# Kernel optimization log

Measured on AMD Instinct MI355X. Metric: run time of the kernel, lower is better.

Reference implementation:

```python
import jax, jax.numpy as jnp
import numpy as np

B, S, D = 128, 256, 768          # batch, seq (pre-sentinel), encoder dim
ARC, TAG = 500, 100              # arc / tag representation dims
LAYERS, TOPK = 2, 8              # config['gnn_layers'], config['top_k']
SP = S + 1                       # seq_len after head sentinel


def setup_inputs() -> dict:
    key = jax.random.key(0)
    ks = jax.random.split(key, 32)
    sc = 0.02
    inp = {
        'inputs': jax.random.normal(ks[0], (B, S, D), jnp.float32),
        'tag_embeddings': jax.random.randint(ks[1], (B, S), 0, 50),
        'mask': jnp.ones((B, S), jnp.int32),
        'head_indices': jax.random.randint(ks[2], (B, S), 0, S),
        'head_tags': jax.random.randint(ks[3], (B, S), 0, 50),
        # parameters
        'head_sentinel': jax.random.normal(ks[4], (D,), jnp.float32),
        'W_ha': jax.random.normal(ks[5], (D, ARC)) * sc, 'b_ha': jnp.zeros((ARC,)),
        'W_da': jax.random.normal(ks[6], (D, ARC)) * sc, 'b_da': jnp.zeros((ARC,)),
        'W_ht': jax.random.normal(ks[7], (D, TAG)) * sc, 'b_ht': jnp.zeros((TAG,)),
        'W_dt': jax.random.normal(ks[8], (D, TAG)) * sc, 'b_dt': jnp.zeros((TAG,)),
        # bilinear attention: use_input_biases=True -> (ARC+1, ARC+1), plus scalar bias
        'bil_W': jax.random.normal(ks[9], (LAYERS + 1, ARC + 1, ARC + 1)) * sc,
        'bil_b': jnp.zeros((LAYERS + 1,)),
        # GCNConv params (PyG: x @ W, symmetric-normalized aggregate, + bias)
        'c1a_W': jax.random.normal(ks[10], (ARC, ARC)) * sc, 'c1a_b': jnp.zeros((ARC,)),
        'c2a_W': jax.random.normal(ks[11], (ARC, ARC)) * sc, 'c2a_b': jnp.zeros((ARC,)),
        'c1r_W': jax.random.normal(ks[12], (TAG, TAG)) * sc, 'c1r_b': jnp.zeros((TAG,)),
        'c2r_W': jax.random.normal(ks[13], (TAG, TAG)) * sc, 'c2r_b': jnp.zeros((TAG,)),
    }
    return inp


def bilinear_attn(m1, m2, W, b):
    # AllenNLP BilinearMatrixAttention with use_input_biases=True
    ones1 = jnp.ones(m1.shape[:-1] + (1,), m1.dtype)
    m1b = jnp.concatenate([m1, ones1], -1)
    m2b = jnp.concatenate([m2, ones1], -1)
    return jnp.einsum('bie,ef,bjf->bij', m1b, W, m2b) + b


def batch_top_k(probs, k):
    # probs: [B, SP, SP] row-softmaxed; edge j(head)->i(dep) for each row's top-k cols,
    # with global (batched) node indexing.
    vals, idx = jax.lax.top_k(probs, k)                      # [B, SP, k]
    offs = (jnp.arange(B) * SP)[:, None, None]
    src = (idx + offs).reshape(-1)
    dst = (jnp.broadcast_to(jnp.arange(SP)[None, :, None], idx.shape) + offs).reshape(-1)
    return src, dst, vals.reshape(-1)


def gcn_conv(x, src, dst, ew, W, b):
    # PyG GCNConv: x@W, add self-loops (weight 1), sym norm, scatter-add at dst, + bias
    N = x.shape[0]
    x = x @ W
    loop = jnp.arange(N)
    row = jnp.concatenate([src, loop])
    col = jnp.concatenate([dst, loop])
    w = jnp.concatenate([ew, jnp.ones((N,), x.dtype)])
    deg = jax.ops.segment_sum(w, col, num_segments=N)
    dinv = jnp.where(deg > 0, jax.lax.rsqrt(deg), 0.0)
    norm = dinv[row] * w * dinv[col]
    out = jax.ops.segment_sum(x[row] * norm[:, None], col, num_segments=N)
    return out + b


def reference(inputs, tag_embeddings, mask, head_indices, head_tags,
              head_sentinel, W_ha, b_ha, W_da, b_da, W_ht, b_ht, W_dt, b_dt,
              bil_W, bil_b, c1a_W, c1a_b, c2a_W, c2a_b, c1r_W, c1r_b, c2r_W, c2r_b):
    elu = jax.nn.elu
    x = jnp.concatenate([jnp.broadcast_to(head_sentinel, (B, 1, D)), inputs], axis=1)  # [B,SP,D]
    head_arc = elu(x @ W_ha + b_ha)
    dept_arc = elu(x @ W_da + b_da)
    head_tag = elu(x @ W_ht + b_ht)
    dep_tag = elu(x @ W_dt + b_dt)

    def two_conv(feat, W1, b1, W2, b2, src, dst, ew):
        h = gcn_conv(feat.reshape(B * SP, -1), src, dst, ew, W1, b1)
        h = gcn_conv(elu(h), src, dst, ew, W2, b2)
        return h.reshape(B, SP, -1)

    for k in range(LAYERS):
        arc_logits = bilinear_attn(head_arc, dept_arc, bil_W[k], bil_b[k])
        arc_probs = jax.nn.softmax(arc_logits, axis=-1)
        src, dst, ew = batch_top_k(arc_probs, TOPK)
        head_arc = two_conv(head_arc, c1a_W, c1a_b, c2a_W, c2a_b, src, dst, ew)
        dept_arc = two_conv(dept_arc, c1a_W, c1a_b, c2a_W, c2a_b, src, dst, ew)
        head_tag = two_conv(head_tag, c1r_W, c1r_b, c2r_W, c2r_b, src, dst, ew)
        dep_tag = two_conv(dep_tag, c1r_W, c1r_b, c2r_W, c2r_b, src, dst, ew)

    arc_logits = bilinear_attn(head_arc, dept_arc, bil_W[-1], bil_b[-1])
    return arc_logits, head_tag, dep_tag
```

## Files before the change

kernel.cpp:

```cpp
#include <hip/hip_runtime.h>
#include <hip/hip_bf16.h>
#include <math.h>
#include <cstddef>

namespace {

constexpr int kB   = 128;
constexpr int kS   = 256;
constexpr int kD   = 768;
constexpr int kSP  = 257;
constexpr int kN   = kB * kSP;
constexpr int kARC = 500;
constexpr int kTAG = 100;
constexpr int KA   = 512;
constexpr int KT   = 128;

typedef __attribute__((ext_vector_type(8))) short short8;
typedef __attribute__((ext_vector_type(4))) float floatx4;
typedef __attribute__((ext_vector_type(2))) float floatx2;
typedef __attribute__((ext_vector_type(4))) unsigned short ushort4v;
typedef __attribute__((ext_vector_type(2))) unsigned short ushort2v;
typedef __hip_bfloat16 bf;

__device__ __forceinline__ float bfval(bf h) { return __bfloat162float(h); }
__device__ __forceinline__ unsigned short bfbits(bf h) {
  unsigned short u; __builtin_memcpy(&u, &h, 2); return u;
}
__device__ __forceinline__ void splitf(float x, bf* h, bf* l) {
  bf hh = __float2bfloat16(x);
  *h = hh;
  *l = __float2bfloat16(x - __bfloat162float(hh));
}

__device__ __forceinline__ void gload16(const bf* g, bf* l) {
  __builtin_amdgcn_global_load_lds(
      (const __attribute__((address_space(1))) void*)g,
      (__attribute__((address_space(3))) void*)l, 16, 0, 0);
}

__global__ void detect_dtype_n(const unsigned* __restrict__ raw, int* __restrict__ flag,
                               int nwords) {
  int lane = threadIdx.x;
  int ok = 0, nz = 0;
  if (lane < nwords) {
    unsigned w = raw[lane];
    if (w != 0u) {
      nz = 1;
      int e = (w >> 7) & 0xFF;
      ok = (e >= 90 && e <= 140);
    }
  }
  unsigned long long ball_ok = __ballot(ok);
  unsigned long long ball_nz = __ballot(nz);
  if (lane == 0) {
    int cok = __popcll(ball_ok), cnz = __popcll(ball_nz);
    flag[0] = (cok * 4 >= cnz * 3) ? 1 : 0;
  }
}

__device__ __forceinline__ float rawload(const void* p, size_t i, int bfm) {
  return bfm ? __bfloat162float(((const bf*)p)[i]) : ((const float*)p)[i];
}

__global__ void conv_off(const void* __restrict__ src, float* __restrict__ dst,
                         int n, long off, const int* __restrict__ flag) {
  int i = blockIdx.x * 256 + threadIdx.x;
  if (i >= n) return;
  dst[i] = rawload(src, (size_t)off + i, *flag);
}

__global__ void wsplit_t(const void* __restrict__ src, const int* __restrict__ flag,
                         long srcOff, int ldsrc, int K, int N, int Kpad,
                         bf* __restrict__ Wh, bf* __restrict__ Wl) {
  long idx = (long)blockIdx.x * 256 + threadIdx.x;
  if (idx >= (long)N * Kpad) return;
  int n = (int)(idx / Kpad), k = (int)(idx % Kpad);
  float v = (k < K) ? rawload(src, (size_t)srcOff + (size_t)k * ldsrc + n, *flag) : 0.f;
  bf h, l;
  splitf(v, &h, &l);
  Wh[idx] = h; Wl[idx] = l;
}

__global__ void xsplit(const void* __restrict__ inp, const void* __restrict__ sent,
                       const int* __restrict__ fi, const int* __restrict__ fs,
                       bf* __restrict__ xh, bf* __restrict__ xl, int g0, int NG) {
  long idx = (long)blockIdx.x * 256 + threadIdx.x;
  long tot = (long)NG * (kD / 4);
  if (idx >= tot) return;
  int n = (int)(idx / (kD / 4));
  int k = (int)(idx % (kD / 4)) * 4;
  int b = n / kSP, r = n - b * kSP;
  const void* src;
  size_t base;
  int bfm;
  if (r == 0) { src = sent; base = (size_t)k; bfm = *fs; }
  else {
    src = inp;
    base = ((size_t)((g0 + b) * kS + (r - 1))) * kD + k;
    bfm = *fi;
  }
  float v[4];
  if (bfm) {
    ushort4v s = *(const ushort4v*)((const unsigned short*)src + base);
#pragma unroll
    for (int j = 0; j < 4; ++j) {
      bf h; unsigned short u = s[j];
      __builtin_memcpy(&h, &u, 2);
      v[j] = __bfloat162float(h);
    }
  } else {
    floatx4 f4 = *(const floatx4*)((const float*)src + base);
#pragma unroll
    for (int j = 0; j < 4; ++j) v[j] = f4[j];
  }
  ushort4v h4, l4;
#pragma unroll
  for (int j = 0; j < 4; ++j) {
    bf h, l;
    splitf(v[j], &h, &l);
    h4[j] = bfbits(h); l4[j] = bfbits(l);
  }
  size_t o = (size_t)n * kD + k;
  *(ushort4v*)((unsigned short*)xh + o) = h4;
  *(ushort4v*)((unsigned short*)xl + o) = l4;
}

constexpr int BM = 128, BN = 128, BK = 32;

template <int EPI, int OUTF32>
__global__ __launch_bounds__(256) void gemm_sp(
    const bf* __restrict__ Ah, const bf* __restrict__ Al, int lda,
    const bf* __restrict__ Bh, const bf* __restrict__ Bl, int ldb,
    bf* __restrict__ Ch, bf* __restrict__ Cl, float* __restrict__ Cf, int ldc,
    int M, int N, int K, const float* __restrict__ bias) {
  __shared__ bf sAh[BM][BK];
  __shared__ bf sAl[BM][BK];
  __shared__ bf sBh[BN][BK];
  __shared__ bf sBl[BN][BK];
  const int tid = threadIdx.x;
  const int lane = tid & 63, wave = tid >> 6;
  const int quad = lane >> 4, l15 = lane & 15;
  const int wm = (wave >> 1) * 64, wn = (wave & 1) * 64;
  const int m0 = blockIdx.x * BM, n0 = blockIdx.y * BN;
  const int lrow = lane >> 2, lkof = (lane & 3) * 8;

  const bf *pAh[2], *pAl[2], *pBh[2], *pBl[2];
#pragma unroll
  for (int jj = 0; jj < 2; ++jj) {
    int rb = wave * 32 + jj * 16;
    int gm = m0 + rb + lrow; if (gm > M - 1) gm = M - 1;
    int gn = n0 + rb + lrow; if (gn > N - 1) gn = N - 1;
    pAh[jj] = Ah + (size_t)gm * lda + lkof;
    pAl[jj] = Al + (size_t)gm * lda + lkof;
    pBh[jj] = Bh + (size_t)gn * ldb + lkof;
    pBl[jj] = Bl + (size_t)gn * ldb + lkof;
  }

  floatx4 acc[4][4] = {};
  for (int k0 = 0; k0 < K; k0 += BK) {
#pragma unroll
    for (int jj = 0; jj < 2; ++jj) {
      const int rb = wave * 32 + jj * 16;
      gload16(pAh[jj] + k0, &sAh[rb][0]);
      gload16(pAl[jj] + k0, &sAl[rb][0]);
      gload16(pBh[jj] + k0, &sBh[rb][0]);
      gload16(pBl[jj] + k0, &sBl[rb][0]);
    }
    __syncthreads();
    short8 a_h[4], a_l[4], b_h[4], b_l[4];
#pragma unroll
    for (int t = 0; t < 4; ++t) {
      a_h[t] = *(const short8*)&sAh[wm + t * 16 + l15][quad * 8];
      a_l[t] = *(const short8*)&sAl[wm + t * 16 + l15][quad * 8];
      b_h[t] = *(const short8*)&sBh[wn + t * 16 + l15][quad * 8];
      b_l[t] = *(const short8*)&sBl[wn + t * 16 + l15][quad * 8];
    }
#pragma unroll
    for (int mt = 0; mt < 4; ++mt)
#pragma unroll
      for (int nt = 0; nt < 4; ++nt) {
        acc[mt][nt] = __builtin_amdgcn_mfma_f32_16x16x32_bf16(a_h[mt], b_h[nt], acc[mt][nt], 0, 0, 0);
        acc[mt][nt] = __builtin_amdgcn_mfma_f32_16x16x32_bf16(a_h[mt], b_l[nt], acc[mt][nt], 0, 0, 0);
        acc[mt][nt] = __builtin_amdgcn_mfma_f32_16x16x32_bf16(a_l[mt], b_h[nt], acc[mt][nt], 0, 0, 0);
      }
    __syncthreads();
  }
#pragma unroll
  for (int mt = 0; mt < 4; ++mt)
#pragma unroll
    for (int reg = 0; reg < 4; ++reg) {
      int m = m0 + wm + mt * 16 + quad * 4 + reg;
      if (m >= M) continue;
#pragma unroll
      for (int nt = 0; nt < 4; ++nt) {
        int n = n0 + wn + nt * 16 + l15;
        if (OUTF32) {
          if (n < N) {
            float v = acc[mt][nt][reg];
            if (EPI >= 1) v += bias[n];
            if (EPI == 1) v = v > 0.f ? v : expm1f(v);
            Cf[(size_t)m * ldc + n] = v;
          }
        } else {
          size_t o = (size_t)m * ldc + n;
          if (n < N) {
            float v = acc[mt][nt][reg];
            if (EPI >= 1) v += bias[n];
            if (EPI == 1) v = v > 0.f ? v : expm1f(v);
            bf h, l;
            splitf(v, &h, &l);
            Ch[o] = h; Cl[o] = l;
          } else if (n < ldc) {
            Ch[o] = __float2bfloat16(0.f);
            Cl[o] = __float2bfloat16(0.f);
          }
        }
      }
    }
}

__global__ __launch_bounds__(256) void bilnt_sp(
    const bf* __restrict__ Th, const bf* __restrict__ Tl,
    const bf* __restrict__ Fh, const bf* __restrict__ Fl,
    float* __restrict__ out, const float* __restrict__ bilb, int bidx,
    int g0, int globOut) {
  __shared__ bf sAh[BM][BK];
  __shared__ bf sAl[BM][BK];
  __shared__ bf sBh[BN][BK];
  __shared__ bf sBl[BN][BK];
  const int z = blockIdx.z;
  const int tid = threadIdx.x;
  const int lane = tid & 63, wave = tid >> 6;
  const int quad = lane >> 4, l15 = lane & 15;
  const int wm = (wave >> 1) * 64, wn = (wave & 1) * 64;
  const int m0 = blockIdx.x * BM, n0 = blockIdx.y * BN;
  const int lrow = lane >> 2, lkof = (lane & 3) * 8;
  const bf* Ah = Th + (size_t)z * kSP * KA;
  const bf* Al = Tl + (size_t)z * kSP * KA;
  const bf* Bh = Fh + (size_t)z * kSP * KA;
  const bf* Bl = Fl + (size_t)z * kSP * KA;

  const bf *pAh[2], *pAl[2], *pBh[2], *pBl[2];
#pragma unroll
  for (int jj = 0; jj < 2; ++jj) {
    int rb = wave * 32 + jj * 16;
    int gm = m0 + rb + lrow; if (gm > kSP - 1) gm = kSP - 1;
    int gn = n0 + rb + lrow; if (gn > kSP - 1) gn = kSP - 1;
    pAh[jj] = Ah + (size_t)gm * KA + lkof;
    pAl[jj] = Al + (size_t)gm * KA + lkof;
    pBh[jj] = Bh + (size_t)gn * KA + lkof;
    pBl[jj] = Bl + (size_t)gn * KA + lkof;
  }

  floatx4 acc[4][4] = {};
  for (int k0 = 0; k0 < KA; k0 += BK) {
#pragma unroll
    for (int jj = 0; jj < 2; ++jj) {
      const int rb = wave * 32 + jj * 16;
      gload16(pAh[jj] + k0, &sAh[rb][0]);
      gload16(pAl[jj] + k0, &sAl[rb][0]);
      gload16(pBh[jj] + k0, &sBh[rb][0]);
      gload16(pBl[jj] + k0, &sBl[rb][0]);
    }
    __syncthreads();
    short8 a_h[4], a_l[4], b_h[4], b_l[4];
#pragma unroll
    for (int t = 0; t < 4; ++t) {
      a_h[t] = *(const short8*)&sAh[wm + t * 16 + l15][quad * 8];
      a_l[t] = *(const short8*)&sAl[wm + t * 16 + l15][quad * 8];
      b_h[t] = *(const short8*)&sBh[wn + t * 16 + l15][quad * 8];
      b_l[t] = *(const short8*)&sBl[wn + t * 16 + l15][quad * 8];
    }
#pragma unroll
    for (int mt = 0; mt < 4; ++mt)
#pragma unroll
      for (int nt = 0; nt < 4; ++nt) {
        acc[mt][nt] = __builtin_amdgcn_mfma_f32_16x16x32_bf16(a_h[mt], b_h[nt], acc[mt][nt], 0, 0, 0);
        acc[mt][nt] = __builtin_amdgcn_mfma_f32_16x16x32_bf16(a_h[mt], b_l[nt], acc[mt][nt], 0, 0, 0);
        acc[mt][nt] = __builtin_amdgcn_mfma_f32_16x16x32_bf16(a_l[mt], b_h[nt], acc[mt][nt], 0, 0, 0);
      }
    __syncthreads();
  }
  const float sb = bilb[bidx];
  const int bb = globOut ? (g0 + z) : z;
#pragma unroll
  for (int mt = 0; mt < 4; ++mt)
#pragma unroll
    for (int reg = 0; reg < 4; ++reg) {
      int i = m0 + wm + mt * 16 + quad * 4 + reg;
      if (i >= kSP) continue;
      float rowterm = bfval(Ah[(size_t)i * KA + 500]) + bfval(Al[(size_t)i * KA + 500]) + sb;
#pragma unroll
      for (int nt = 0; nt < 4; ++nt) {
        int j = n0 + wn + nt * 16 + l15;
        if (j >= kSP) continue;
        out[((size_t)bb * kSP + i) * kSP + j] = acc[mt][nt][reg] + rowterm;
      }
    }
}

__global__ void softmax_topk(const float* __restrict__ logits,
                             int* __restrict__ idx8,
                             float* __restrict__ val8,
                             float* __restrict__ dinv) {
  const int row = blockIdx.x;
  const int lane = threadIdx.x;
  const int rowbase = row - (row % kSP);
  const float* L = logits + (size_t)row * kSP;
  float v[5];
  int c[5];
#pragma unroll
  for (int q = 0; q < 5; ++q) {
    int j = lane + q * 64;
    c[q] = j;
    v[q] = (j < kSP) ? L[j] : -INFINITY;
  }
  float m = v[0];
#pragma unroll
  for (int q = 1; q < 5; ++q) m = fmaxf(m, v[q]);
  for (int off = 32; off > 0; off >>= 1) m = fmaxf(m, __shfl_xor(m, off));
  float s = 0.f;
#pragma unroll
  for (int q = 0; q < 5; ++q) s += expf(v[q] - m);
  for (int off = 32; off > 0; off >>= 1) s += __shfl_xor(s, off);
  const float invs = 1.f / s;
  float degsum = 0.f;
  for (int t = 0; t < 8; ++t) {
    float bvv = -INFINITY;
    int bii = kSP;
#pragma unroll
    for (int q = 0; q < 5; ++q)
      if (v[q] > bvv) { bvv = v[q]; bii = c[q]; }
    for (int off = 32; off > 0; off >>= 1) {
      float ov = __shfl_xor(bvv, off);
      int oi = __shfl_xor(bii, off);
      if (ov > bvv || (ov == bvv && oi < bii)) { bvv = ov; bii = oi; }
    }
    float p = expf(bvv - m) * invs;
    degsum += p;
    if (lane == 0) { idx8[row * 8 + t] = rowbase + bii; val8[row * 8 + t] = p; }
#pragma unroll
    for (int q = 0; q < 5; ++q)
      if (c[q] == bii) v[q] = -INFINITY;
  }
  if (lane == 0) dinv[row] = 1.f / sqrtf(1.f + degsum);
}

template <int ELU, int OUTF32>
__global__ void gcn_agg(const float* __restrict__ Y, int ldy, int F,
                        const int* __restrict__ idx8, const float* __restrict__ val8,
                        const float* __restrict__ dinv, const float* __restrict__ bias,
                        bf* __restrict__ Zh, bf* __restrict__ Zl,
                        float* __restrict__ Zf, int ldzf) {
  const int n = blockIdx.x;
  __shared__ float w[9];
  __shared__ int srcs[8];
  const int t = threadIdx.x;
  if (t < 8) {
    int s = idx8[n * 8 + t];
    srcs[t] = s;
    w[t] = dinv[n] * val8[n * 8 + t] * dinv[s];
  } else if (t == 8) {
    float di = dinv[n];
    w[8] = di * di;
  }
  __syncthreads();
  const int lim = OUTF32 ? F : ldy;
  for (int f = t * 2; f < lim; f += (int)blockDim.x * 2) {
    size_t on = (size_t)n * ldy + f;
    if (!OUTF32 && f >= F) {
      ushort2v zz = {0, 0};
      *(ushort2v*)((unsigned short*)Zh + on) = zz;
      *(ushort2v*)((unsigned short*)Zl + on) = zz;
      continue;
    }
    floatx2 y0 = *(const floatx2*)(Y + on);
    float a0 = w[8] * y0[0], a1 = w[8] * y0[1];
#pragma unroll
    for (int e = 0; e < 8; ++e) {
      floatx2 ys = *(const floatx2*)(Y + (size_t)srcs[e] * ldy + f);
      a0 += w[e] * ys[0];
      a1 += w[e] * ys[1];
    }
    a0 += bias[f];
    a1 += bias[f + 1];
    if (ELU) {
      a0 = a0 > 0.f ? a0 : expm1f(a0);
      a1 = a1 > 0.f ? a1 : expm1f(a1);
    }
    if (OUTF32) {
      floatx2 o = {a0, a1};
      *(floatx2*)(Zf + (size_t)n * ldzf + f) = o;
    } else {
      bf h0, l0, h1, l1;
      splitf(a0, &h0, &l0);
      splitf(a1, &h1, &l1);
      ushort2v hv = {bfbits(h0), bfbits(h1)};
      ushort2v lv = {bfbits(l0), bfbits(l1)};
      *(ushort2v*)((unsigned short*)Zh + on) = hv;
      *(ushort2v*)((unsigned short*)Zl + on) = lv;
    }
  }
}

}

extern "C" void kernel_launch(void* const* d_in, const int* in_sizes, int n_in,
                              void* d_out, int out_size, void* d_ws, size_t ws_size,
                              hipStream_t stream) {
  (void)out_size;

  const int roleSize[20] = {kB * kS * kD, kD,
                            kD * kARC, kARC, kD * kARC, kARC,
                            kD * kTAG, kTAG, kD * kTAG, kTAG,
                            3 * 501 * 501, 3,
                            kARC * kARC, kARC, kARC * kARC, kARC,
                            kTAG * kTAG, kTAG, kTAG * kTAG, kTAG};
  const int roleOcc[20]  = {0, 0, 0, 0, 1, 1, 0, 0, 1, 1, 0, 0,
                            0, 2, 1, 3, 0, 2, 1, 3};
  int roleIdx[20] = {0, 5, 6, 7, 8, 9, 10, 11, 12, 13, 14, 15,
                     16, 17, 18, 19, 20, 21, 22, 23};
  for (int r = 0; r < 20; ++r) {
    int occ = 0, found = -1;
    for (int i = 0; i < n_in; ++i) {
      if (in_sizes[i] == roleSize[r]) {
        if (occ == roleOcc[r]) { found = i; break; }
        ++occ;
      }
    }
    if (found >= 0) roleIdx[r] = found;
    else if (roleIdx[r] >= n_in) roleIdx[r] = 0;
  }
  const void* src_of[20];
  for (int r = 0; r < 20; ++r) src_of[r] = d_in[roleIdx[r]];

  auto need_bytes = [](int GB) -> size_t {
    size_t NG = (size_t)GB * kSP, s = 0;
    auto al = [&](size_t b) { s += (b + 255) & ~(size_t)255; };
    al(256);
    for (int i = 0; i < 4; ++i) al((size_t)kARC * kD * 2);
    for (int i = 0; i < 4; ++i) al((size_t)kTAG * kD * 2);
    al(kARC * 4); al(kARC * 4); al(kTAG * 4); al(kTAG * 4);
    for (int i = 0; i < 6; ++i) al((size_t)501 * KA * 2);
    al(3 * 501 * 4); al(256);
    for (int i = 0; i < 4; ++i) al((size_t)kARC * KA * 2);
    for (int i = 0; i < 4; ++i) al((size_t)kTAG * KT * 2);
    al(kARC * 4); al(kARC * 4); al(kTAG * 4); al(kTAG * 4);
    al(NG * kD * 2); al(NG * kD * 2);
    for (int i = 0; i < 4; ++i) al(NG * KA * 2);
    for (int i = 0; i < 4; ++i) al(NG * KT * 2);
    al(NG * KA * 2); al(NG * KA * 2);
    al(NG * KA * 4);
    al(NG * kSP * 4);
    al(NG * 8 * 4); al(NG * 8 * 4); al(NG * 4);
    return s;
  };
  int GB = 1;
  for (int cand : {128, 64, 32, 16, 8, 4, 2, 1})
    if (need_bytes(cand) <= ws_size) { GB = cand; break; }
  const int G = kB / GB;
  const int NG = GB * kSP;
  const int mb = (NG + BM - 1) / BM;

  char* ws = (char*)d_ws;
  size_t off = 0;
  auto alloc = [&](size_t bytes) -> void* {
    void* p = ws + off;
    off += (bytes + 255) & ~(size_t)255;
    return p;
  };
  int* flags = (int*)alloc(256);
  bf *WtHAh = (bf*)alloc((size_t)kARC * kD * 2), *WtHAl = (bf*)alloc((size_t)kARC * kD * 2);
  bf *WtDAh = (bf*)alloc((size_t)kARC * kD * 2), *WtDAl = (bf*)alloc((size_t)kARC * kD * 2);
  bf *WtHTh = (bf*)alloc((size_t)kTAG * kD * 2), *WtHTl = (bf*)alloc((size_t)kTAG * kD * 2);
  bf *WtDTh = (bf*)alloc((size_t)kTAG * kD * 2), *WtDTl = (bf*)alloc((size_t)kTAG * kD * 2);
  float* bha = (float*)alloc(kARC * 4);
  float* bda = (float*)alloc(kARC * 4);
  float* bht = (float*)alloc(kTAG * 4);
  float* bdt = (float*)alloc(kTAG * 4);
  bf* bilWh[3]; bf* bilWl[3];
  for (int k = 0; k < 3; ++k) {
    bilWh[k] = (bf*)alloc((size_t)501 * KA * 2);
    bilWl[k] = (bf*)alloc((size_t)501 * KA * 2);
  }
  float* brow = (float*)alloc(3 * 501 * 4);
  float* bilbf = (float*)alloc(256);
  bf *c1ah = (bf*)alloc((size_t)kARC * KA * 2), *c1al = (bf*)alloc((size_t)kARC * KA * 2);
  bf *c2ah = (bf*)alloc((size_t)kARC * KA * 2), *c2al = (bf*)alloc((size_t)kARC * KA * 2);
  bf *c1rh = (bf*)alloc((size_t)kTAG * KT * 2), *c1rl = (bf*)alloc((size_t)kTAG * KT * 2);
  bf *c2rh = (bf*)alloc((size_t)kTAG * KT * 2), *c2rl = (bf*)alloc((size_t)kTAG * KT * 2);
  float* c1ab = (float*)alloc(kARC * 4);
  float* c2ab = (float*)alloc(kARC * 4);
  float* c1rb = (float*)alloc(kTAG * 4);
  float* c2rb = (float*)alloc(kTAG * 4);
  bf *xh = (bf*)alloc((size_t)NG * kD * 2), *xl = (bf*)alloc((size_t)NG * kD * 2);
  bf *fHAh = (bf*)alloc((size_t)NG * KA * 2), *fHAl = (bf*)alloc((size_t)NG * KA * 2);
  bf *fDAh = (bf*)alloc((size_t)NG * KA * 2), *fDAl = (bf*)alloc((size_t)NG * KA * 2);
  bf *fHTh = (bf*)alloc((size_t)NG * KT * 2), *fHTl = (bf*)alloc((size_t)NG * KT * 2);
  bf *fDTh = (bf*)alloc((size_t)NG * KT * 2), *fDTl = (bf*)alloc((size_t)NG * KT * 2);
  bf *Yh = (bf*)alloc((size_t)NG * KA * 2), *Yl = (bf*)alloc((size_t)NG * KA * 2);
  float* Yf = (float*)alloc((size_t)NG * KA * 4);
  float* logits = (float*)alloc((size_t)NG * kSP * 4);
  int*   idx8 = (int*)alloc((size_t)NG * 8 * 4);
  float* val8 = (float*)alloc((size_t)NG * 8 * 4);
  float* dinv = (float*)alloc((size_t)NG * 4);

  for (int r = 0; r < 20; ++r) {
    int n = roleSize[r];
    int nwords = n / 4; if (nwords < 1) nwords = 1; if (nwords > 64) nwords = 64;
    detect_dtype_n<<<1, 64, 0, stream>>>((const unsigned*)src_of[r], flags + r, nwords);
  }
  auto cvt = [&](int role, float* dst, int n, long o) {
    conv_off<<<(n + 255) / 256, 256, 0, stream>>>(src_of[role], dst, n, o, flags + role);
  };
  cvt(3, bha, kARC, 0); cvt(5, bda, kARC, 0); cvt(7, bht, kTAG, 0); cvt(9, bdt, kTAG, 0);
  cvt(11, bilbf, 3, 0);
  cvt(13, c1ab, kARC, 0); cvt(15, c2ab, kARC, 0); cvt(17, c1rb, kTAG, 0); cvt(19, c2rb, kTAG, 0);
  auto wsp = [&](int role, long o, int ldsrc, int K, int N, int Kpad, bf* Wh, bf* Wl) {
    long tot = (long)N * Kpad;
    wsplit_t<<<(int)((tot + 255) / 256), 256, 0, stream>>>(src_of[role], flags + role, o,
                                                           ldsrc, K, N, Kpad, Wh, Wl);
  };
  wsp(2, 0, kARC, kD, kARC, kD, WtHAh, WtHAl);
  wsp(4, 0, kARC, kD, kARC, kD, WtDAh, WtDAl);
  wsp(6, 0, kTAG, kD, kTAG, kD, WtHTh, WtHTl);
  wsp(8, 0, kTAG, kD, kTAG, kD, WtDTh, WtDTl);
  for (int k = 0; k < 3; ++k) {
    wsp(10, (long)k * 501 * 501, 501, 500, 501, KA, bilWh[k], bilWl[k]);
    cvt(10, brow + k * 501, 501, (long)k * 501 * 501 + 500 * 501);
  }
  wsp(12, 0, kARC, kARC, kARC, KA, c1ah, c1al);
  wsp(14, 0, kARC, kARC, kARC, KA, c2ah, c2al);
  wsp(16, 0, kTAG, kTAG, kTAG, KT, c1rh, c1rl);
  wsp(18, 0, kTAG, kTAG, kTAG, KT, c2rh, c2rl);

  float* outp = (float*)d_out;
  const size_t arc_elems = (size_t)kB * kSP * kSP;

  for (int g = 0; g < G; ++g) {
    const int g0 = g * GB;

    {
      long tot = (long)NG * (kD / 4);
      xsplit<<<(int)((tot + 255) / 256), 256, 0, stream>>>(
          src_of[0], src_of[1], flags + 0, flags + 1, xh, xl, g0, NG);
    }
    gemm_sp<1, 0><<<dim3(mb, 4), 256, 0, stream>>>(xh, xl, kD, WtHAh, WtHAl, kD,
                                                   fHAh, fHAl, nullptr, KA, NG, kARC, kD, bha);
    gemm_sp<1, 0><<<dim3(mb, 4), 256, 0, stream>>>(xh, xl, kD, WtDAh, WtDAl, kD,
                                                   fDAh, fDAl, nullptr, KA, NG, kARC, kD, bda);
    gemm_sp<1, 0><<<dim3(mb, 1), 256, 0, stream>>>(xh, xl, kD, WtHTh, WtHTl, kD,
                                                   fHTh, fHTl, nullptr, KT, NG, kTAG, kD, bht);
    gemm_sp<1, 0><<<dim3(mb, 1), 256, 0, stream>>>(xh, xl, kD, WtDTh, WtDTl, kD,
                                                   fDTh, fDTl, nullptr, KT, NG, kTAG, kD, bdt);

    for (int k = 0; k < 2; ++k) {
      gemm_sp<2, 0><<<dim3(mb, 4), 256, 0, stream>>>(fHAh, fHAl, KA, bilWh[k], bilWl[k], KA,
                                                     Yh, Yl, nullptr, KA, NG, 501, KA,
                                                     brow + k * 501);
      bilnt_sp<<<dim3(3, 3, GB), 256, 0, stream>>>(Yh, Yl, fDAh, fDAl, logits, bilbf, k, g0, 0);
      softmax_topk<<<NG, 64, 0, stream>>>(logits, idx8, val8, dinv);

      bf* fh[2] = {fHAh, fDAh};
      bf* fl[2] = {fHAl, fDAl};
      for (int ff = 0; ff < 2; ++ff) {
        gemm_sp<0, 1><<<dim3(mb, 4), 256, 0, stream>>>(fh[ff], fl[ff], KA, c1ah, c1al, KA,
                                                       nullptr, nullptr, Yf, KA, NG, kARC, KA,
                                                       nullptr);
        gcn_agg<1, 0><<<NG, 256, 0, stream>>>(Yf, KA, kARC, idx8, val8, dinv, c1ab,
                                              Yh, Yl, nullptr, 0);
        gemm_sp<0, 1><<<dim3(mb, 4), 256, 0, stream>>>(Yh, Yl, KA, c2ah, c2al, KA,
                                                       nullptr, nullptr, Yf, KA, NG, kARC, KA,
                                                       nullptr);
        gcn_agg<0, 0><<<NG, 256, 0, stream>>>(Yf, KA, kARC, idx8, val8, dinv, c2ab,
                                              fh[ff], fl[ff], nullptr, 0);
      }
      bf* th[2] = {fHTh, fDTh};
      bf* tl[2] = {fHTl, fDTl};
      for (int ff = 0; ff < 2; ++ff) {
        gemm_sp<0, 1><<<dim3(mb, 1), 256, 0, stream>>>(th[ff], tl[ff], KT, c1rh, c1rl, KT,
                                                       nullptr, nullptr, Yf, KT, NG, kTAG, KT,
                                                       nullptr);
        gcn_agg<1, 0><<<NG, 64, 0, stream>>>(Yf, KT, kTAG, idx8, val8, dinv, c1rb,
                                             Yh, Yl, nullptr, 0);
        gemm_sp<0, 1><<<dim3(mb, 1), 256, 0, stream>>>(Yh, Yl, KT, c2rh, c2rl, KT,
                                                       nullptr, nullptr, Yf, KT, NG, kTAG, KT,
                                                       nullptr);
        if (k == 1) {
          float* dst = outp + arc_elems + (ff == 1 ? (size_t)kN * kTAG : 0)
                       + (size_t)g0 * kSP * kTAG;
          gcn_agg<0, 1><<<NG, 64, 0, stream>>>(Yf, KT, kTAG, idx8, val8, dinv, c2rb,
                                               nullptr, nullptr, dst, kTAG);
        } else {
          gcn_agg<0, 0><<<NG, 64, 0, stream>>>(Yf, KT, kTAG, idx8, val8, dinv, c2rb,
                                               th[ff], tl[ff], nullptr, 0);
        }
      }
    }

    gemm_sp<2, 0><<<dim3(mb, 4), 256, 0, stream>>>(fHAh, fHAl, KA, bilWh[2], bilWl[2], KA,
                                                   Yh, Yl, nullptr, KA, NG, 501, KA,
                                                   brow + 2 * 501);
    bilnt_sp<<<dim3(3, 3, GB), 256, 0, stream>>>(Yh, Yl, fDAh, fDAl, outp, bilbf, 2, g0, 1);
  }
}
```

Baseline: 3.405 ms.

## Double-buffer shared-memory tiles in split-bf16 GEMM and bilinear kernels

Both MFMA GEMM kernels now keep two LDS buffers per operand. The next K-slice is prefetched into the alternate buffer right after the barrier, while the MFMAs run on the current one, and the trailing barrier is dropped. The aim is to hide global-load latency behind compute and halve the number of barriers per K step. In exchange LDS use doubles to 64KB per block, which may lower occupancy. Correctness relies on gload16 being an async direct-to-LDS load that waits at the next barrier.

```diff
diff --git a/kernel.cpp b/kernel.cpp
--- a/kernel.cpp
+++ b/kernel.cpp
@@ -133,10 +133,10 @@
     const bf* __restrict__ Bh, const bf* __restrict__ Bl, int ldb,
     bf* __restrict__ Ch, bf* __restrict__ Cl, float* __restrict__ Cf, int ldc,
     int M, int N, int K, const float* __restrict__ bias) {
-  __shared__ bf sAh[BM][BK];
-  __shared__ bf sAl[BM][BK];
-  __shared__ bf sBh[BN][BK];
-  __shared__ bf sBl[BN][BK];
+  __shared__ bf sAh[2][BM][BK];
+  __shared__ bf sAl[2][BM][BK];
+  __shared__ bf sBh[2][BN][BK];
+  __shared__ bf sBl[2][BN][BK];
   const int tid = threadIdx.x;
   const int lane = tid & 63, wave = tid >> 6;
   const int quad = lane >> 4, l15 = lane & 15;
@@ -145,35 +145,41 @@
   const int lrow = lane >> 2, lkof = (lane & 3) * 8;
 
   const bf *pAh[2], *pAl[2], *pBh[2], *pBl[2];
+  int rb[2];
 #pragma unroll
   for (int jj = 0; jj < 2; ++jj) {
-    int rb = wave * 32 + jj * 16;
-    int gm = m0 + rb + lrow; if (gm > M - 1) gm = M - 1;
-    int gn = n0 + rb + lrow; if (gn > N - 1) gn = N - 1;
+    rb[jj] = wave * 32 + jj * 16;
+    int gm = m0 + rb[jj] + lrow; if (gm > M - 1) gm = M - 1;
+    int gn = n0 + rb[jj] + lrow; if (gn > N - 1) gn = N - 1;
     pAh[jj] = Ah + (size_t)gm * lda + lkof;
     pAl[jj] = Al + (size_t)gm * lda + lkof;
     pBh[jj] = Bh + (size_t)gn * ldb + lkof;
     pBl[jj] = Bl + (size_t)gn * ldb + lkof;
   }
 
+  auto stage = [&](int bi, int k0) {
+#pragma unroll
+    for (int jj = 0; jj < 2; ++jj) {
+      gload16(pAh[jj] + k0, &sAh[bi][rb[jj]][0]);
+      gload16(pAl[jj] + k0, &sAl[bi][rb[jj]][0]);
+      gload16(pBh[jj] + k0, &sBh[bi][rb[jj]][0]);
+      gload16(pBl[jj] + k0, &sBl[bi][rb[jj]][0]);
+    }
+  };
+
   floatx4 acc[4][4] = {};
+  stage(0, 0);
+  int cur = 0;
   for (int k0 = 0; k0 < K; k0 += BK) {
-#pragma unroll
-    for (int jj = 0; jj < 2; ++jj) {
-      const int rb = wave * 32 + jj * 16;
-      gload16(pAh[jj] + k0, &sAh[rb][0]);
-      gload16(pAl[jj] + k0, &sAl[rb][0]);
-      gload16(pBh[jj] + k0, &sBh[rb][0]);
-      gload16(pBl[jj] + k0, &sBl[rb][0]);
-    }
     __syncthreads();
+    if (k0 + BK < K) stage(cur ^ 1, k0 + BK);
     short8 a_h[4], a_l[4], b_h[4], b_l[4];
 #pragma unroll
     for (int t = 0; t < 4; ++t) {
-      a_h[t] = *(const short8*)&sAh[wm + t * 16 + l15][quad * 8];
-      a_l[t] = *(const short8*)&sAl[wm + t * 16 + l15][quad * 8];
-      b_h[t] = *(const short8*)&sBh[wn + t * 16 + l15][quad * 8];
-      b_l[t] = *(const short8*)&sBl[wn + t * 16 + l15][quad * 8];
+      a_h[t] = *(const short8*)&sAh[cur][wm + t * 16 + l15][quad * 8];
+      a_l[t] = *(const short8*)&sAl[cur][wm + t * 16 + l15][quad * 8];
+      b_h[t] = *(const short8*)&sBh[cur][wn + t * 16 + l15][quad * 8];
+      b_l[t] = *(const short8*)&sBl[cur][wn + t * 16 + l15][quad * 8];
     }
 #pragma unroll
     for (int mt = 0; mt < 4; ++mt)
@@ -183,7 +189,7 @@
         acc[mt][nt] = __builtin_amdgcn_mfma_f32_16x16x32_bf16(a_h[mt], b_l[nt], acc[mt][nt], 0, 0, 0);
         acc[mt][nt] = __builtin_amdgcn_mfma_f32_16x16x32_bf16(a_l[mt], b_h[nt], acc[mt][nt], 0, 0, 0);
       }
-    __syncthreads();
+    cur ^= 1;
   }
 #pragma unroll
   for (int mt = 0; mt < 4; ++mt)
@@ -224,10 +230,10 @@
     const bf* __restrict__ Fh, const bf* __restrict__ Fl,
     float* __restrict__ out, const float* __restrict__ bilb, int bidx,
     int g0, int globOut) {
-  __shared__ bf sAh[BM][BK];
-  __shared__ bf sAl[BM][BK];
-  __shared__ bf sBh[BN][BK];
-  __shared__ bf sBl[BN][BK];
+  __shared__ bf sAh[2][BM][BK];
+  __shared__ bf sAl[2][BM][BK];
+  __shared__ bf sBh[2][BN][BK];
+  __shared__ bf sBl[2][BN][BK];
   const int z = blockIdx.z;
   const int tid = threadIdx.x;
   const int lane = tid & 63, wave = tid >> 6;
@@ -241,35 +247,41 @@
   const bf* Bl = Fl + (size_t)z * kSP * KA;
 
   const bf *pAh[2], *pAl[2], *pBh[2], *pBl[2];
+  int rb[2];
 #pragma unroll
   for (int jj = 0; jj < 2; ++jj) {
-    int rb = wave * 32 + jj * 16;
-    int gm = m0 + rb + lrow; if (gm > kSP - 1) gm = kSP - 1;
-    int gn = n0 + rb + lrow; if (gn > kSP - 1) gn = kSP - 1;
+    rb[jj] = wave * 32 + jj * 16;
+    int gm = m0 + rb[jj] + lrow; if (gm > kSP - 1) gm = kSP - 1;
+    int gn = n0 + rb[jj] + lrow; if (gn > kSP - 1) gn = kSP - 1;
     pAh[jj] = Ah + (size_t)gm * KA + lkof;
     pAl[jj] = Al + (size_t)gm * KA + lkof;
     pBh[jj] = Bh + (size_t)gn * KA + lkof;
     pBl[jj] = Bl + (size_t)gn * KA + lkof;
   }
 
+  auto stage = [&](int bi, int k0) {
+#pragma unroll
+    for (int jj = 0; jj < 2; ++jj) {
+      gload16(pAh[jj] + k0, &sAh[bi][rb[jj]][0]);
+      gload16(pAl[jj] + k0, &sAl[bi][rb[jj]][0]);
+      gload16(pBh[jj] + k0, &sBh[bi][rb[jj]][0]);
+      gload16(pBl[jj] + k0, &sBl[bi][rb[jj]][0]);
+    }
+  };
+
   floatx4 acc[4][4] = {};
+  stage(0, 0);
+  int cur = 0;
   for (int k0 = 0; k0 < KA; k0 += BK) {
-#pragma unroll
-    for (int jj = 0; jj < 2; ++jj) {
-      const int rb = wave * 32 + jj * 16;
-      gload16(pAh[jj] + k0, &sAh[rb][0]);
-      gload16(pAl[jj] + k0, &sAl[rb][0]);
-      gload16(pBh[jj] + k0, &sBh[rb][0]);
-      gload16(pBl[jj] + k0, &sBl[rb][0]);
-    }
     __syncthreads();
+    if (k0 + BK < KA) stage(cur ^ 1, k0 + BK);
     short8 a_h[4], a_l[4], b_h[4], b_l[4];
 #pragma unroll
     for (int t = 0; t < 4; ++t) {
-      a_h[t] = *(const short8*)&sAh[wm + t * 16 + l15][quad * 8];
-      a_l[t] = *(const short8*)&sAl[wm + t * 16 + l15][quad * 8];
-      b_h[t] = *(const short8*)&sBh[wn + t * 16 + l15][quad * 8];
-      b_l[t] = *(const short8*)&sBl[wn + t * 16 + l15][quad * 8];
+      a_h[t] = *(const short8*)&sAh[cur][wm + t * 16 + l15][quad * 8];
+      a_l[t] = *(const short8*)&sAl[cur][wm + t * 16 + l15][quad * 8];
+      b_h[t] = *(const short8*)&sBh[cur][wn + t * 16 + l15][quad * 8];
+      b_l[t] = *(const short8*)&sBl[cur][wn + t * 16 + l15][quad * 8];
     }
 #pragma unroll
     for (int mt = 0; mt < 4; ++mt)
@@ -279,7 +291,7 @@
         acc[mt][nt] = __builtin_amdgcn_mfma_f32_16x16x32_bf16(a_h[mt], b_l[nt], acc[mt][nt], 0, 0, 0);
         acc[mt][nt] = __builtin_amdgcn_mfma_f32_16x16x32_bf16(a_l[mt], b_h[nt], acc[mt][nt], 0, 0, 0);
       }
-    __syncthreads();
+    cur ^= 1;
   }
   const float sb = bilb[bidx];
   const int bb = globOut ? (g0 + z) : z;
```

Measured after the change: 3.395 ms. Within noise of the previous version (-0.3%).
